# Kernel optimization log

Hardware: AMD Instinct MI355X
Metric: run time of the kernel (lower is better)

Reference implementation:

```python
import jax, jax.numpy as jnp
import numpy as np

N_NODES = 100000
N_EDGES = 3200000
N_GRAPHS = 64


def setup_inputs() -> dict:
    key = jax.random.key(0)
    ks = jax.random.split(key, 16)
    s = 0.1
    pos = jax.random.normal(ks[0], (N_NODES, 2), dtype=jnp.float32) * 100.0
    w1a = jax.random.normal(ks[1], (4, 32), dtype=jnp.float32) * s
    b1a = jax.random.normal(ks[2], (32,), dtype=jnp.float32) * s
    w1b = jax.random.normal(ks[3], (32, 32), dtype=jnp.float32) * s
    b1b = jax.random.normal(ks[4], (32,), dtype=jnp.float32) * s
    w2a = jax.random.normal(ks[5], (34, 32), dtype=jnp.float32) * s
    b2a = jax.random.normal(ks[6], (32,), dtype=jnp.float32) * s
    w2b = jax.random.normal(ks[7], (32, 32), dtype=jnp.float32) * s
    b2b = jax.random.normal(ks[8], (32,), dtype=jnp.float32) * s
    wc = jax.random.normal(ks[9], (32, 3), dtype=jnp.float32) * s
    bc = jax.random.normal(ks[10], (3,), dtype=jnp.float32) * s
    edge_index = jax.random.randint(ks[11], (2, N_EDGES), 0, N_NODES, dtype=jnp.int64)
    batch = jnp.sort(jax.random.randint(ks[12], (N_NODES,), 0, N_GRAPHS, dtype=jnp.int64))
    return {"pos": pos, "w1a": w1a, "b1a": b1a, "w1b": w1b, "b1b": b1b,
            "w2a": w2a, "b2a": b2a, "w2b": w2b, "b2b": b2b,
            "wc": wc, "bc": bc, "edge_index": edge_index, "batch": batch}


def _seg_max0(x, seg, n):
    # segment max with empty segments filled with 0 (PyG scatter-max semantics)
    m = jax.ops.segment_max(x, seg, num_segments=n)
    return jnp.where(jnp.isfinite(m), m, 0.0)


def _pointnet_layer(h, pos, src, dst, w1, b1, w2, b2):
    # message: mlp(cat[h_j, pos_j - pos_i]); aggr: max over incoming edges at i
    x = jnp.concatenate([h[src], pos[src] - pos[dst]], axis=-1)  # [E, C+2]
    m = jnp.maximum(x @ w1 + b1, 0.0) @ w2 + b2                   # [E, 32]
    return _seg_max0(m, dst, N_NODES)                             # [N, 32]


def reference(pos, w1a, b1a, w1b, b1b, w2a, b2a, w2b, b2b, wc, bc,
              edge_index, batch):
    src, dst = edge_index[0], edge_index[1]  # messages flow src(j) -> dst(i)
    h = jax.nn.relu(_pointnet_layer(pos, pos, src, dst, w1a, b1a, w1b, b1b))
    h = jax.nn.relu(_pointnet_layer(h, pos, src, dst, w2a, b2a, w2b, b2b))
    g = _seg_max0(h, batch, N_GRAPHS)        # global max pool per graph
    return g @ wc + bc                        # [G, 3]
```

## Files before the change

### kernel.cpp

```cpp
#include <hip/hip_runtime.h>
#include <hip/hip_bf16.h>


#define NEG_BIG (-3.0e38f)
#define BSHIFT 9
#define NBMAX 256
#define CHUNKS 16384
#define CAP 32512
#define RCAP 16384

typedef __attribute__((ext_vector_type(8))) short short8;
typedef __attribute__((ext_vector_type(4))) float f32x4;
typedef __attribute__((ext_vector_type(4))) unsigned uint4v;

__device__ __forceinline__ short bf16r(float f) {
    unsigned u = __float_as_uint(f);
    unsigned r = (u + 0x7FFFu + ((u >> 16) & 1u)) >> 16;
    return (short)r;
}
__device__ __forceinline__ unsigned pack_bf16(float lo, float hi) {
    return ((unsigned)(unsigned short)bf16r(lo)) |
           (((unsigned)(unsigned short)bf16r(hi)) << 16);
}

__global__ __launch_bounds__(256) void pre1_kernel(
    const float* __restrict__ pos, const float* __restrict__ w1a,
    const float* __restrict__ b1a, const float* __restrict__ w1b,
    const float* __restrict__ w2b, unsigned* __restrict__ Abf,
    unsigned* __restrict__ Bbf, unsigned* __restrict__ wfbuf,
    float* __restrict__ h1, float* __restrict__ h2, int N)
{
    if (blockIdx.x == gridDim.x - 1) {
        int t = threadIdx.x;
        int l = t >> 7, frag = (t >> 6) & 1, lane = t & 63;
        const float* w = l ? w2b : w1b;
        int m16 = lane & 15, kq = (lane >> 4) * 8;
        int cb = frag * 16 + m16;
        unsigned out[4];
#pragma unroll
        for (int p = 0; p < 4; ++p)
            out[p] = pack_bf16(w[(kq + 2 * p) * 32 + cb],
                               w[(kq + 2 * p + 1) * 32 + cb]);
        *(uint4v*)(wfbuf + (size_t)t * 4) = (uint4v){out[0], out[1], out[2], out[3]};
        return;
    }
    int t = blockIdx.x * 256 + threadIdx.x;
    if (t >= N * 16) return;
    int n = t >> 4, c0 = (t & 15) * 2;
    float px = pos[2 * n], py = pos[2 * n + 1];
    float a[2], b[2];
#pragma unroll
    for (int i = 0; i < 2; ++i) {
        int c = c0 + i;
        float w0 = w1a[c], w1 = w1a[32 + c], w2 = w1a[64 + c], w3 = w1a[96 + c];
        a[i] = fmaf(px, w0 + w2, fmaf(py, w1 + w3, b1a[c]));
        b[i] = -(px * w2 + py * w3);
    }
    Abf[t] = pack_bf16(a[0], a[1]);
    Bbf[t] = pack_bf16(b[0], b[1]);
    *(float2*)(h1 + 2 * (size_t)t) = make_float2(0.0f, 0.0f);
    *(float2*)(h2 + 2 * (size_t)t) = make_float2(0.0f, 0.0f);
}

__global__ __launch_bounds__(256) void pre2_kernel(
    const float* __restrict__ pos, const float* __restrict__ h1,
    const float* __restrict__ w2a, const float* __restrict__ b2a,
    unsigned* __restrict__ Abf, unsigned* __restrict__ Bbf, int N)
{
    int n = blockIdx.x * 256 + threadIdx.x;
    if (n >= N) return;
    float px = pos[2 * n], py = pos[2 * n + 1];
    const float4* hq = (const float4*)(h1 + (size_t)n * 32);
    float4 hv[8];
#pragma unroll
    for (int q = 0; q < 8; ++q) hv[q] = hq[q];
    float acc[32];
#pragma unroll
    for (int c = 0; c < 32; ++c)
        acc[c] = fmaf(px, w2a[1024 + c], fmaf(py, w2a[1056 + c], b2a[c]));
    const float* hf = (const float*)hv;
#pragma unroll
    for (int k = 0; k < 32; ++k) {
        float hk = hf[k];
#pragma unroll
        for (int c = 0; c < 32; ++c) acc[c] = fmaf(hk, w2a[k * 32 + c], acc[c]);
    }
    unsigned* Arow = Abf + (size_t)n * 16;
    unsigned* Brow = Bbf + (size_t)n * 16;
#pragma unroll
    for (int p = 0; p < 16; ++p) {
        Arow[p] = pack_bf16(acc[2 * p], acc[2 * p + 1]);
        Brow[p] = pack_bf16(-(px * w2a[1024 + 2 * p] + py * w2a[1056 + 2 * p]),
                            -(px * w2a[1025 + 2 * p] + py * w2a[1057 + 2 * p]));
    }
}

__global__ __launch_bounds__(1024) void bucket_scatter_kernel(
    const int* __restrict__ ei, int* __restrict__ bcnt,
    int* __restrict__ csr_tmp, int E, int NB)
{
    __shared__ int lh[NBMAX];
    __shared__ int lb[NBMAX];
    int tid = threadIdx.x;
    for (int i = tid; i < NB; i += 1024) lh[i] = 0;
    __syncthreads();
    const int* dsts = ei + E;
    int base0 = blockIdx.x * CHUNKS;
    int4 sv[4], dv[4];
#pragma unroll
    for (int j = 0; j < 4; ++j) {
        int e = base0 + tid * 4 + j * 4096;
        if (e + 3 < E) {
            sv[j] = *(const int4*)(ei + e);
            dv[j] = *(const int4*)(dsts + e);
        } else {
            int s0 = 0, s1 = 0, s2 = 0, s3 = 0;
            int d0 = -1, d1 = -1, d2 = -1, d3 = -1;
            if (e < E)     { s0 = ei[e];     d0 = dsts[e]; }
            if (e + 1 < E) { s1 = ei[e + 1]; d1 = dsts[e + 1]; }
            if (e + 2 < E) { s2 = ei[e + 2]; d2 = dsts[e + 2]; }
            sv[j] = make_int4(s0, s1, s2, s3);
            dv[j] = make_int4(d0, d1, d2, d3);
        }
        if (dv[j].x >= 0) atomicAdd(&lh[dv[j].x >> BSHIFT], 1);
        if (dv[j].y >= 0) atomicAdd(&lh[dv[j].y >> BSHIFT], 1);
        if (dv[j].z >= 0) atomicAdd(&lh[dv[j].z >> BSHIFT], 1);
        if (dv[j].w >= 0) atomicAdd(&lh[dv[j].w >> BSHIFT], 1);
    }
    __syncthreads();
    for (int i = tid; i < NB; i += 1024) {
        int c = lh[i];
        if (c) {
            int o = atomicAdd(bcnt + i, c);
            if (o > CAP - c) o = CAP - c;
            lb[i] = i * CAP + o;
        }
    }
    __syncthreads();
    for (int i = tid; i < NB; i += 1024) lh[i] = 0;
    __syncthreads();
#pragma unroll
    for (int j = 0; j < 4; ++j) {
        int s, d, b, o;
        s = sv[j].x; d = dv[j].x;
        if (d >= 0) { b = d >> BSHIFT; o = atomicAdd(&lh[b], 1);
                      csr_tmp[lb[b] + o] = s | ((d & 511) << 20); }
        s = sv[j].y; d = dv[j].y;
        if (d >= 0) { b = d >> BSHIFT; o = atomicAdd(&lh[b], 1);
                      csr_tmp[lb[b] + o] = s | ((d & 511) << 20); }
        s = sv[j].z; d = dv[j].z;
        if (d >= 0) { b = d >> BSHIFT; o = atomicAdd(&lh[b], 1);
                      csr_tmp[lb[b] + o] = s | ((d & 511) << 20); }
        s = sv[j].w; d = dv[j].w;
        if (d >= 0) { b = d >> BSHIFT; o = atomicAdd(&lh[b], 1);
                      csr_tmp[lb[b] + o] = s | ((d & 511) << 20); }
    }
}

__global__ __launch_bounds__(1024) void place_kernel(
    const int* __restrict__ csr_tmp, const int* __restrict__ bcnt,
    int* __restrict__ pcur, int* __restrict__ csr_src,
    int* __restrict__ tile_dst, int N)
{
    __shared__ int rec_cache[RCAP];
    __shared__ int cnt[512], pre[512], cur[512];
    __shared__ int pstart_s;
    int b = blockIdx.x, tid = threadIdx.x;
    int d0 = b << BSHIFT;
    int start = b * CAP;
    int len = bcnt[b];
    if (len > CAP) len = CAP;
    if (tid < 512) cnt[tid] = 0;
    __syncthreads();
    for (int i = tid; i < len; i += 1024) {
        int rec = csr_tmp[start + i];
        if (i < RCAP) rec_cache[i] = rec;
        atomicAdd(&cnt[rec >> 20], 1);
    }
    __syncthreads();
    if (tid < 64) {
        int lane = tid;
        int a[8];
        int s = 0;
#pragma unroll
        for (int j = 0; j < 8; ++j) {
            a[j] = (cnt[8 * lane + j] + 15) & ~15;
            s += a[j];
        }
        int x = s;
#pragma unroll
        for (int d = 1; d < 64; d <<= 1) {
            int t = __shfl_up(x, d, 64);
            if (lane >= d) x += t;
        }
        int total = __shfl(x, 63, 64);
        if (lane == 0) pstart_s = total ? atomicAdd(pcur, total) : 0;
        int run = x - s;
#pragma unroll
        for (int j = 0; j < 8; ++j) {
            pre[8 * lane + j] = run;
            cur[8 * lane + j] = run;
            run += a[j];
        }
    }
    __syncthreads();
    int pstart = pstart_s;
    for (int i = tid; i < len; i += 1024) {
        int rec = (i < RCAP) ? rec_cache[i] : csr_tmp[start + i];
        int p = atomicAdd(&cur[rec >> 20], 1);
        csr_src[pstart + p] = rec & 0xFFFFF;
    }
    if (tid < 512) {
        int d = d0 + tid;
        if (d < N) {
            int c = cnt[tid], pc = (c + 15) & ~15;
            int base = pstart + pre[tid];
            for (int k = c; k < pc; ++k) csr_src[base + k] = -1;
            int tb = base >> 4, nt = pc >> 4;
            for (int k = 0; k < nt; ++k) tile_dst[tb + k] = d;
        }
    }
}

__global__ __launch_bounds__(256, 4) void edge_layer_kernel(
    const int* __restrict__ csr_src, const int* __restrict__ tile_dst,
    const unsigned* __restrict__ Abf, const unsigned* __restrict__ Bbf,
    const unsigned* __restrict__ wf, const float* __restrict__ bias,
    unsigned int* __restrict__ hout)
{
    int tid = threadIdx.x;
    int lane = tid & 63;
    int wv = tid >> 6;
    int wbase = blockIdx.x * 256 + wv * 64;
    int m16 = lane & 15;
    int q = lane >> 4;
    int kq = q * 8;
    int ch = (lane < 16) ? m16 : (16 + m16);

    int td[4];
#pragma unroll
    for (int eg = 0; eg < 4; ++eg) td[eg] = tile_dst[(wbase >> 4) + eg];
    if (td[0] < 0 && td[1] < 0 && td[2] < 0 && td[3] < 0) return;

    short8 bf0 = __builtin_bit_cast(short8, *(const uint4v*)(wf + (size_t)lane * 4));
    short8 bf1 = __builtin_bit_cast(short8, *(const uint4v*)(wf + (size_t)(64 + lane) * 4));
    float myb = bias[ch];
    unsigned int* hch = hout + ch;

    int src[4];
#pragma unroll
    for (int eg = 0; eg < 4; ++eg) {
        int sidx = wbase + eg * 16 + m16;
        src[eg] = (td[eg] >= 0) ? csr_src[sidx] : -1;
    }

    uint4v ua4[4], ub4[4];
#pragma unroll
    for (int eg = 0; eg < 4; ++eg) {
        int brow = (td[eg] >= 0) ? td[eg] : 0;
        int arow = (src[eg] >= 0) ? src[eg] : brow;
        ua4[eg] = *(const uint4v*)(Abf + (size_t)arow * 16 + (kq >> 1));
        ub4[eg] = *(const uint4v*)(Bbf + (size_t)brow * 16 + (kq >> 1));
    }

    f32x4 zero = {0.0f, 0.0f, 0.0f, 0.0f};
    float cv0 = NEG_BIG, cv1 = NEG_BIG;
    int cdst = -1;
#pragma unroll
    for (int eg = 0; eg < 4; ++eg) {
        unsigned long long bal = __ballot(src[eg] >= 0);
        uint4v pk;
#pragma unroll
        for (int d = 0; d < 4; ++d) {
            unsigned uad = ua4[eg][d], ubd = ub4[eg][d];
            float a0 = __uint_as_float(uad << 16);
            float a1 = __uint_as_float(uad & 0xFFFF0000u);
            float b0 = __uint_as_float(ubd << 16);
            float b1 = __uint_as_float(ubd & 0xFFFF0000u);
            float r0 = fmaxf(a0 + b0, 0.0f);
            float r1 = fmaxf(a1 + b1, 0.0f);
            pk[d] = __builtin_amdgcn_perm(__float_as_uint(r1),
                                          __float_as_uint(r0), 0x07060302u);
        }
        short8 af = __builtin_bit_cast(short8, pk);
        f32x4 d0 = __builtin_amdgcn_mfma_f32_16x16x32_bf16(af, bf0, zero, 0, 0, 0);
        f32x4 d1 = __builtin_amdgcn_mfma_f32_16x16x32_bf16(af, bf1, zero, 0, 0, 0);
        float v0, v1;
        if (bal == ~0ull) {
            v0 = fmaxf(fmaxf(d0[0], d0[1]), fmaxf(d0[2], d0[3]));
            v1 = fmaxf(fmaxf(d1[0], d1[1]), fmaxf(d1[2], d1[3]));
        } else {
            v0 = NEG_BIG; v1 = NEG_BIG;
#pragma unroll
            for (int r = 0; r < 4; ++r) {
                bool ok = (bal >> (q * 4 + r)) & 1ull;
                v0 = fmaxf(v0, ok ? d0[r] : NEG_BIG);
                v1 = fmaxf(v1, ok ? d1[r] : NEG_BIG);
            }
        }
        v0 = fmaxf(v0, __shfl_xor(v0, 16, 64));
        v0 = fmaxf(v0, __shfl_xor(v0, 32, 64));
        v1 = fmaxf(v1, __shfl_xor(v1, 16, 64));
        v1 = fmaxf(v1, __shfl_xor(v1, 32, 64));
        int d = td[eg];
        if (d != cdst) {
            if (cdst >= 0 && lane < 32) {
                float x = ((lane < 16) ? cv0 : cv1) + myb;
                if (x > 0.0f)
                    atomicMax(hch + (size_t)cdst * 32, __float_as_uint(x));
            }
            cdst = d; cv0 = v0; cv1 = v1;
        } else {
            cv0 = fmaxf(cv0, v0); cv1 = fmaxf(cv1, v1);
        }
    }
    if (cdst >= 0 && lane < 32) {
        float x = ((lane < 16) ? cv0 : cv1) + myb;
        if (x > 0.0f)
            atomicMax(hch + (size_t)cdst * 32, __float_as_uint(x));
    }
}

__global__ __launch_bounds__(256) void pool_kernel(
    const float* __restrict__ h2, const int* __restrict__ batch,
    unsigned int* __restrict__ gbuf, int N)
{
    int g = blockIdx.x, p = blockIdx.y;
    __shared__ int sbound[2];
    __shared__ float red[256];
    if (threadIdx.x < 2) {
        int target = g + (int)threadIdx.x;
        int lo = 0, hi = N;
        while (lo < hi) {
            int mid = (lo + hi) >> 1;
            if (batch[mid] < target) lo = mid + 1; else hi = mid;
        }
        sbound[threadIdx.x] = lo;
    }
    __syncthreads();
    int start = sbound[0], end = sbound[1];
    int c = threadIdx.x & 31, r = threadIdx.x >> 5;
    float mx = 0.0f;
    for (int n = start + p * 8 + r; n < end; n += 128)
        mx = fmaxf(mx, h2[(size_t)n * 32 + c]);
    red[threadIdx.x] = mx;
    __syncthreads();
    if (r < 4) red[threadIdx.x] = fmaxf(red[threadIdx.x], red[threadIdx.x + 128]);
    __syncthreads();
    if (r < 2) red[threadIdx.x] = fmaxf(red[threadIdx.x], red[threadIdx.x + 64]);
    __syncthreads();
    if (r == 0) {
        float v = fmaxf(red[threadIdx.x], red[threadIdx.x + 32]);
        if (v > 0.0f) atomicMax(gbuf + g * 32 + c, __float_as_uint(v));
    }
}

__global__ __launch_bounds__(192) void out_kernel(
    const float* __restrict__ gbuf, const float* __restrict__ wc,
    const float* __restrict__ bc, float* __restrict__ out, int G)
{
    int t = threadIdx.x;
    if (t >= G * 3) return;
    int g = t / 3, j = t % 3;
    float s = bc[j];
#pragma unroll
    for (int c = 0; c < 32; ++c)
        s = fmaf(gbuf[g * 32 + c], wc[c * 3 + j], s);
    out[t] = s;
}

extern "C" void kernel_launch(void* const* d_in, const int* in_sizes, int n_in,
                              void* d_out, int out_size, void* d_ws, size_t ws_size,
                              hipStream_t stream) {
    const float* pos = (const float*)d_in[0];
    const float* w1a = (const float*)d_in[1];
    const float* b1a = (const float*)d_in[2];
    const float* w1b = (const float*)d_in[3];
    const float* b1b = (const float*)d_in[4];
    const float* w2a = (const float*)d_in[5];
    const float* b2a = (const float*)d_in[6];
    const float* w2b = (const float*)d_in[7];
    const float* b2b = (const float*)d_in[8];
    const float* wc  = (const float*)d_in[9];
    const float* bc  = (const float*)d_in[10];
    const int* ei    = (const int*)d_in[11];
    const int* batch = (const int*)d_in[12];

    const int N = in_sizes[12];
    const int E = in_sizes[11] / 2;
    const int G = out_size / 3;
    const size_t NC = (size_t)N * 32;
    const int NB = (N + 511) >> BSHIFT;
    const int SMAX = (E + 15 * ((N < E) ? N : E) + 255) & ~255;
    const int TMAX = SMAX >> 4;

    int* bcnt    = (int*)d_ws;
    int* pcur    = bcnt + 256;
    float* gbuf  = (float*)(pcur + 256);
    unsigned* wfbuf = (unsigned*)(gbuf + 2048);
    int* csr_src = (int*)(wfbuf + 1024);
    int* tile_dst = csr_src + SMAX;
    unsigned* Abf = (unsigned*)(tile_dst + TMAX);
    unsigned* Bbf = Abf + (size_t)N * 16;
    float* h1    = (float*)(Bbf + (size_t)N * 16);
    float* h2    = h1 + NC;
    int* csr_tmp = (int*)h1;

    int npBlocks = ((int)(N * 16) + 255) / 256 + 1;
    int nBlocks  = (N + 255) / 256;
    int sBlocks  = (E + CHUNKS - 1) / CHUNKS;
    int edBlocks = (SMAX + 255) / 256;

    hipMemsetAsync(bcnt, 0, (512 + 2048) * sizeof(int), stream);
    hipMemsetAsync(tile_dst, 0xFF, (size_t)TMAX * sizeof(int), stream);

    bucket_scatter_kernel<<<sBlocks, 1024, 0, stream>>>(ei, bcnt, csr_tmp, E, NB);
    place_kernel<<<NB, 1024, 0, stream>>>(csr_tmp, bcnt, pcur,
                                          csr_src, tile_dst, N);
    pre1_kernel<<<npBlocks, 256, 0, stream>>>(pos, w1a, b1a, w1b, w2b,
                                              Abf, Bbf, wfbuf, h1, h2, N);
    edge_layer_kernel<<<edBlocks, 256, 0, stream>>>(csr_src, tile_dst, Abf, Bbf,
                                                    wfbuf, b1b, (unsigned int*)h1);
    pre2_kernel<<<nBlocks, 256, 0, stream>>>(pos, h1, w2a, b2a, Abf, Bbf, N);
    edge_layer_kernel<<<edBlocks, 256, 0, stream>>>(csr_src, tile_dst, Abf, Bbf,
                                                    wfbuf + 512, b2b,
                                                    (unsigned int*)h2);
    pool_kernel<<<dim3(G, 16), 256, 0, stream>>>(h2, batch,
                                                 (unsigned int*)gbuf, N);
    out_kernel<<<1, 192, 0, stream>>>(gbuf, wc, bc, (float*)d_out, G);
}
```

Measured before the change: 280.1 us.

## Fuse tile_dst init and output projection, halve scatter chunk, raise edge occupancy

Folds the tile_dst memset into the bucket-scatter kernel and fuses the final output projection into the pool kernel using a last-block atomic counter, removing two launches. Halves the edges handled per scatter block so more blocks run in parallel. Raises the edge-layer minimum-blocks launch bound from 4 to 8, which may force register spilling. The last-block pattern relies on the reused counter word being zeroed by the existing memset.

```diff
diff --git a/kernel.cpp b/kernel.cpp
--- a/kernel.cpp
+++ b/kernel.cpp
@@ -5,7 +5,7 @@
 #define NEG_BIG (-3.0e38f)
 #define BSHIFT 9
 #define NBMAX 256
-#define CHUNKS 16384
+#define CHUNKS 8192
 #define CAP 32512
 #define RCAP 16384
 
@@ -97,18 +97,21 @@
 
 __global__ __launch_bounds__(1024) void bucket_scatter_kernel(
     const int* __restrict__ ei, int* __restrict__ bcnt,
-    int* __restrict__ csr_tmp, int E, int NB)
+    int* __restrict__ csr_tmp, int* __restrict__ tile_dst,
+    int E, int NB, int TMAX)
 {
     __shared__ int lh[NBMAX];
     __shared__ int lb[NBMAX];
     int tid = threadIdx.x;
     for (int i = tid; i < NB; i += 1024) lh[i] = 0;
+    for (int i = blockIdx.x * 1024 + tid; i < TMAX; i += gridDim.x * 1024)
+        tile_dst[i] = -1;
     __syncthreads();
     const int* dsts = ei + E;
     int base0 = blockIdx.x * CHUNKS;
-    int4 sv[4], dv[4];
-#pragma unroll
-    for (int j = 0; j < 4; ++j) {
+    int4 sv[2], dv[2];
+#pragma unroll
+    for (int j = 0; j < 2; ++j) {
         int e = base0 + tid * 4 + j * 4096;
         if (e + 3 < E) {
             sv[j] = *(const int4*)(ei + e);
@@ -140,7 +143,7 @@
     for (int i = tid; i < NB; i += 1024) lh[i] = 0;
     __syncthreads();
 #pragma unroll
-    for (int j = 0; j < 4; ++j) {
+    for (int j = 0; j < 2; ++j) {
         int s, d, b, o;
         s = sv[j].x; d = dv[j].x;
         if (d >= 0) { b = d >> BSHIFT; o = atomicAdd(&lh[b], 1);
@@ -222,7 +225,7 @@
     }
 }
 
-__global__ __launch_bounds__(256, 4) void edge_layer_kernel(
+__global__ __launch_bounds__(256, 8) void edge_layer_kernel(
     const int* __restrict__ csr_src, const int* __restrict__ tile_dst,
     const unsigned* __restrict__ Abf, const unsigned* __restrict__ Bbf,
     const unsigned* __restrict__ wf, const float* __restrict__ bias,
@@ -323,11 +326,14 @@
 
 __global__ __launch_bounds__(256) void pool_kernel(
     const float* __restrict__ h2, const int* __restrict__ batch,
-    unsigned int* __restrict__ gbuf, int N)
+    unsigned int* __restrict__ gbuf, const float* __restrict__ wc,
+    const float* __restrict__ bc, float* __restrict__ out,
+    int* __restrict__ done, int N, int G)
 {
     int g = blockIdx.x, p = blockIdx.y;
     __shared__ int sbound[2];
     __shared__ float red[256];
+    __shared__ int last_s;
     if (threadIdx.x < 2) {
         int target = g + (int)threadIdx.x;
         int lo = 0, hi = N;
@@ -353,20 +359,26 @@
         float v = fmaxf(red[threadIdx.x], red[threadIdx.x + 32]);
         if (v > 0.0f) atomicMax(gbuf + g * 32 + c, __float_as_uint(v));
     }
-}
-
-__global__ __launch_bounds__(192) void out_kernel(
-    const float* __restrict__ gbuf, const float* __restrict__ wc,
-    const float* __restrict__ bc, float* __restrict__ out, int G)
-{
-    int t = threadIdx.x;
-    if (t >= G * 3) return;
-    int g = t / 3, j = t % 3;
-    float s = bc[j];
-#pragma unroll
-    for (int c = 0; c < 32; ++c)
-        s = fmaf(gbuf[g * 32 + c], wc[c * 3 + j], s);
-    out[t] = s;
+    __syncthreads();
+    if (threadIdx.x == 0) {
+        __threadfence();
+        int prev = atomicAdd(done, 1);
+        last_s = (prev == G * 16 - 1);
+    }
+    __syncthreads();
+    if (last_s) {
+        int t = threadIdx.x;
+        if (t < G * 3) {
+            int gg = t / 3, j = t % 3;
+            float s = bc[j];
+#pragma unroll
+            for (int cc = 0; cc < 32; ++cc) {
+                unsigned u = atomicOr(gbuf + gg * 32 + cc, 0u);
+                s = fmaf(__uint_as_float(u), wc[cc * 3 + j], s);
+            }
+            out[t] = s;
+        }
+    }
 }
 
 extern "C" void kernel_launch(void* const* d_in, const int* in_sizes, int n_in,
@@ -412,9 +424,9 @@
     int edBlocks = (SMAX + 255) / 256;
 
     hipMemsetAsync(bcnt, 0, (512 + 2048) * sizeof(int), stream);
-    hipMemsetAsync(tile_dst, 0xFF, (size_t)TMAX * sizeof(int), stream);
-
-    bucket_scatter_kernel<<<sBlocks, 1024, 0, stream>>>(ei, bcnt, csr_tmp, E, NB);
+
+    bucket_scatter_kernel<<<sBlocks, 1024, 0, stream>>>(ei, bcnt, csr_tmp,
+                                                        tile_dst, E, NB, TMAX);
     place_kernel<<<NB, 1024, 0, stream>>>(csr_tmp, bcnt, pcur,
                                           csr_src, tile_dst, N);
     pre1_kernel<<<npBlocks, 256, 0, stream>>>(pos, w1a, b1a, w1b, w2b,
@@ -426,6 +438,7 @@
                                                     wfbuf + 512, b2b,
                                                     (unsigned int*)h2);
     pool_kernel<<<dim3(G, 16), 256, 0, stream>>>(h2, batch,
-                                                 (unsigned int*)gbuf, N);
-    out_kernel<<<1, 192, 0, stream>>>(gbuf, wc, bc, (float*)d_out, G);
-}
+                                                 (unsigned int*)gbuf,
+                                                 wc, bc, (float*)d_out,
+                                                 pcur + 1, N, G);
+}
```

Measured after the change: 303.3 us. +8.3%, slower.
